# Performance work log

Measured on AMD Instinct MI355X. Metric: run time of the kernel, lower is better.

Reference implementation:

```python
import jax, jax.numpy as jnp
import numpy as np

ORIG_IN = 4096
ORIG_OUT = 4096
ACTIVE = 2048
RANK = 16
SCALING = 32.0 / 16.0  # lora_alpha / r


def setup_inputs() -> dict:
    key = jax.random.key(0)
    ks = jax.random.split(key, 7)
    x = jax.random.normal(ks[0], (2, 4096, ORIG_IN), dtype=jnp.float32)
    W_base = jax.random.normal(ks[1], (ACTIVE, ACTIVE), dtype=jnp.float32) * 0.02
    b_base = jax.random.normal(ks[2], (ACTIVE,), dtype=jnp.float32) * 0.02
    lora_A = jax.random.normal(ks[3], (RANK, ACTIVE), dtype=jnp.float32) * 0.02
    # lora_B is zero-initialized in the module, but use small random values so
    # the LoRA path contributes non-trivially to the baseline computation.
    lora_B = jax.random.normal(ks[4], (ACTIVE, RANK), dtype=jnp.float32) * 0.02
    # sorted unique index subsets (pruning masks)
    in_indices = jnp.sort(jax.random.permutation(ks[5], ORIG_IN)[:ACTIVE]).astype(jnp.int32)
    out_indices = jnp.sort(jax.random.permutation(ks[6], ORIG_OUT)[:ACTIVE]).astype(jnp.int32)
    return {
        "x": x, "W_base": W_base, "b_base": b_base,
        "lora_A": lora_A, "lora_B": lora_B,
        "in_indices": in_indices, "out_indices": out_indices,
    }


def reference(x, W_base, b_base, lora_A, lora_B, in_indices, out_indices):
    batch_dims = x.shape[:-1]
    x_flat = x.reshape(-1, ORIG_IN)            # [N, orig_in]
    x_sel = x_flat[:, in_indices]              # gather -> [N, active]
    # LoRA path: (x @ A^T) @ B^T * scaling  (dropout = identity, eval mode)
    lora_out = jnp.einsum('na,ra->nr', x_sel, lora_A)
    lora_out = jnp.einsum('nr,or->no', lora_out, lora_B) * SCALING
    # Base pruned linear
    base_out = jnp.einsum('na,oa->no', x_sel, W_base) + b_base
    combined = base_out + lora_out             # [N, active]
    # Scatter into zero-initialized full output
    out_flat = jnp.zeros((x_flat.shape[0], ORIG_OUT), dtype=combined.dtype)
    out_flat = out_flat.at[:, out_indices].set(combined)
    return out_flat.reshape(batch_dims + (ORIG_OUT,))
```

## Files before the change

### kernel.cpp

```cpp
#include <hip/hip_runtime.h>
#include <hip/hip_bf16.h>
#include <stdint.h>

#define M_DIM 8192
#define K_DIM 2048
#define N_DIM 2048
#define IN_DIM 4096
#define OUT_DIM 4096
#define SCALING 2.0f

typedef __attribute__((ext_vector_type(8))) short bf16x8_t;
typedef __attribute__((ext_vector_type(4))) float f32x4_t;

__device__ __forceinline__ void load_lds16(const void* gptr, void* lptr) {
    __builtin_amdgcn_global_load_lds(
        (const __attribute__((address_space(1))) uint32_t*)(uintptr_t)gptr,
        (__attribute__((address_space(3))) uint32_t*)(uintptr_t)lptr,
        16, 0, 0);
}

__global__ void fold_w_kernel(const float* __restrict__ Wb,
                              const float* __restrict__ lA,
                              const float* __restrict__ lB,
                              __hip_bfloat16* __restrict__ We) {
    const int k = blockIdx.x * 256 + threadIdx.x;
    const int o = blockIdx.y;
    float acc = Wb[(size_t)o * K_DIM + k];
    #pragma unroll
    for (int r = 0; r < 16; ++r)
        acc += SCALING * lB[o * 16 + r] * lA[r * K_DIM + k];
    We[(size_t)o * K_DIM + k] = __float2bfloat16(acc);
}

__global__ void gather_cast_kernel(const float* __restrict__ x,
                                   const int* __restrict__ idx,
                                   __hip_bfloat16* __restrict__ xs) {
    const int n = blockIdx.x;
    const int c0 = threadIdx.x * 8;
    const float* xrow = x + (size_t)n * IN_DIM;
    int4 i0 = *(const int4*)(idx + c0);
    int4 i1 = *(const int4*)(idx + c0 + 4);
    union { bf16x8_t v; __hip_bfloat16 h[8]; } u;
    u.h[0] = __float2bfloat16(xrow[i0.x]);
    u.h[1] = __float2bfloat16(xrow[i0.y]);
    u.h[2] = __float2bfloat16(xrow[i0.z]);
    u.h[3] = __float2bfloat16(xrow[i0.w]);
    u.h[4] = __float2bfloat16(xrow[i1.x]);
    u.h[5] = __float2bfloat16(xrow[i1.y]);
    u.h[6] = __float2bfloat16(xrow[i1.z]);
    u.h[7] = __float2bfloat16(xrow[i1.w]);
    *(bf16x8_t*)(xs + (size_t)n * K_DIM + c0) = u.v;
}

__global__ void __launch_bounds__(256, 2)
gemm_scatter_kernel(const __hip_bfloat16* __restrict__ A,
                    const __hip_bfloat16* __restrict__ B,
                    const float* __restrict__ bias,
                    const int* __restrict__ oidx,
                    float* __restrict__ out)
{
    __shared__ __hip_bfloat16 As[128 * 64];
    __shared__ __hip_bfloat16 Bs[128 * 64];

    const int tid  = threadIdx.x;
    const int wave = tid >> 6;
    const int lane = tid & 63;
    const int m0 = blockIdx.y * 128;
    const int n0 = blockIdx.x * 128;

    const int wm = (wave >> 1) * 64;
    const int wn = (wave & 1) * 64;

    const int srow  = tid >> 3;
    const int sslot = tid & 7;

    const int r15 = lane & 15;
    const int qd  = lane >> 4;

    f32x4_t acc[4][4] = {};

    for (int k0 = 0; k0 < K_DIM; k0 += 64) {
        #pragma unroll
        for (int it = 0; it < 4; ++it) {
            const int row = it * 32 + srow;
            const int q = sslot ^ (row & 7);
            const __hip_bfloat16* ga = A + (size_t)(m0 + row) * K_DIM + k0 + q * 8;
            const __hip_bfloat16* gb = B + (size_t)(n0 + row) * K_DIM + k0 + q * 8;
            load_lds16(ga, (void*)&As[(it * 32 + wave * 8) * 64]);
            load_lds16(gb, (void*)&Bs[(it * 32 + wave * 8) * 64]);
        }
        __syncthreads();

        #pragma unroll
        for (int s = 0; s < 2; ++s) {
            bf16x8_t af[4], bfr[4];
            #pragma unroll
            for (int i = 0; i < 4; ++i) {
                const int rowa = wm + i * 16 + r15;
                const int pa = (s * 4 + qd) ^ (rowa & 7);
                af[i] = *(const bf16x8_t*)&As[rowa * 64 + pa * 8];
                const int rowb = wn + i * 16 + r15;
                const int pb = (s * 4 + qd) ^ (rowb & 7);
                bfr[i] = *(const bf16x8_t*)&Bs[rowb * 64 + pb * 8];
            }
            #pragma unroll
            for (int i = 0; i < 4; ++i)
                #pragma unroll
                for (int j = 0; j < 4; ++j)
                    acc[i][j] = __builtin_amdgcn_mfma_f32_16x16x32_bf16(
                        af[i], bfr[j], acc[i][j], 0, 0, 0);
        }
        __syncthreads();
    }

    #pragma unroll
    for (int j = 0; j < 4; ++j) {
        const int gn = n0 + wn + j * 16 + r15;
        const int oc = oidx[gn];
        const float bv = bias[gn];
        #pragma unroll
        for (int i = 0; i < 4; ++i) {
            const int gm = m0 + wm + i * 16 + qd * 4;
            #pragma unroll
            for (int r = 0; r < 4; ++r)
                out[(size_t)(gm + r) * OUT_DIM + oc] = acc[i][j][r] + bv;
        }
    }
}

extern "C" void kernel_launch(void* const* d_in, const int* in_sizes, int n_in,
                              void* d_out, int out_size, void* d_ws, size_t ws_size,
                              hipStream_t stream) {
    const float* x      = (const float*)d_in[0];
    const float* W_base = (const float*)d_in[1];
    const float* b_base = (const float*)d_in[2];
    const float* lora_A = (const float*)d_in[3];
    const float* lora_B = (const float*)d_in[4];
    const int* in_idx   = (const int*)d_in[5];
    const int* out_idx  = (const int*)d_in[6];
    float* out = (float*)d_out;

    __hip_bfloat16* xs = (__hip_bfloat16*)d_ws;
    __hip_bfloat16* We = (__hip_bfloat16*)((char*)d_ws + (size_t)M_DIM * K_DIM * 2);

    hipMemsetAsync(d_out, 0, (size_t)M_DIM * OUT_DIM * sizeof(float), stream);

    fold_w_kernel<<<dim3(K_DIM / 256, N_DIM), 256, 0, stream>>>(W_base, lora_A, lora_B, We);
    gather_cast_kernel<<<M_DIM, 256, 0, stream>>>(x, in_idx, xs);
    gemm_scatter_kernel<<<dim3(N_DIM / 128, M_DIM / 128), 256, 0, stream>>>(
        xs, We, b_base, out_idx, out);
}
```

Baseline: 371.7 us.

## Write compact bf16 GEMM output then scatter via inverse index map, dropping memset

The GEMM now writes its result into a compact bf16 buffer instead of scattering fp32 values directly into the wide output. A new kernel builds an inverse column map by binary search, and a scatter kernel writes every output element exactly once with coalesced float4 stores, inserting zeros for unmapped columns. This removes the full-output memset and the strided scattered stores. The gather kernel also stages each input row into LDS with coalesced loads before indexing. The cost is an extra bf16 round-trip of the result, which also lowers output precision, and the old path remains as a fallback when workspace is too small.

```diff
diff --git a/kernel.cpp b/kernel.cpp
--- a/kernel.cpp
+++ b/kernel.cpp
@@ -32,32 +32,53 @@
     We[(size_t)o * K_DIM + k] = __float2bfloat16(acc);
 }
 
-__global__ void gather_cast_kernel(const float* __restrict__ x,
-                                   const int* __restrict__ idx,
-                                   __hip_bfloat16* __restrict__ xs) {
+__global__ void __launch_bounds__(256)
+gather_cast_kernel(const float* __restrict__ x,
+                   const int* __restrict__ idx,
+                   __hip_bfloat16* __restrict__ xs) {
+    __shared__ float row[IN_DIM];
     const int n = blockIdx.x;
+    const float* xrow = x + (size_t)n * IN_DIM;
+    #pragma unroll
+    for (int i = 0; i < 4; ++i) {
+        const int c = (i * 256 + threadIdx.x) * 4;
+        *(float4*)&row[c] = *(const float4*)&xrow[c];
+    }
+    __syncthreads();
     const int c0 = threadIdx.x * 8;
-    const float* xrow = x + (size_t)n * IN_DIM;
     int4 i0 = *(const int4*)(idx + c0);
     int4 i1 = *(const int4*)(idx + c0 + 4);
     union { bf16x8_t v; __hip_bfloat16 h[8]; } u;
-    u.h[0] = __float2bfloat16(xrow[i0.x]);
-    u.h[1] = __float2bfloat16(xrow[i0.y]);
-    u.h[2] = __float2bfloat16(xrow[i0.z]);
-    u.h[3] = __float2bfloat16(xrow[i0.w]);
-    u.h[4] = __float2bfloat16(xrow[i1.x]);
-    u.h[5] = __float2bfloat16(xrow[i1.y]);
-    u.h[6] = __float2bfloat16(xrow[i1.z]);
-    u.h[7] = __float2bfloat16(xrow[i1.w]);
+    u.h[0] = __float2bfloat16(row[i0.x]);
+    u.h[1] = __float2bfloat16(row[i0.y]);
+    u.h[2] = __float2bfloat16(row[i0.z]);
+    u.h[3] = __float2bfloat16(row[i0.w]);
+    u.h[4] = __float2bfloat16(row[i1.x]);
+    u.h[5] = __float2bfloat16(row[i1.y]);
+    u.h[6] = __float2bfloat16(row[i1.z]);
+    u.h[7] = __float2bfloat16(row[i1.w]);
     *(bf16x8_t*)(xs + (size_t)n * K_DIM + c0) = u.v;
 }
 
+__global__ void build_inv_kernel(const int* __restrict__ oidx,
+                                 int* __restrict__ inv) {
+    const int c = blockIdx.x * 256 + threadIdx.x;
+    int lo = 0, hi = N_DIM;
+    while (lo < hi) {
+        const int mid = (lo + hi) >> 1;
+        if (oidx[mid] < c) lo = mid + 1; else hi = mid;
+    }
+    inv[c] = (lo < N_DIM && oidx[lo] == c) ? lo : -1;
+}
+
+template <bool COMPACT>
 __global__ void __launch_bounds__(256, 2)
-gemm_scatter_kernel(const __hip_bfloat16* __restrict__ A,
-                    const __hip_bfloat16* __restrict__ B,
-                    const float* __restrict__ bias,
-                    const int* __restrict__ oidx,
-                    float* __restrict__ out)
+gemm_kernel(const __hip_bfloat16* __restrict__ A,
+            const __hip_bfloat16* __restrict__ B,
+            const float* __restrict__ bias,
+            const int* __restrict__ oidx,
+            float* __restrict__ out,
+            __hip_bfloat16* __restrict__ Cc)
 {
     __shared__ __hip_bfloat16 As[128 * 64];
     __shared__ __hip_bfloat16 Bs[128 * 64];
@@ -116,16 +137,43 @@
     #pragma unroll
     for (int j = 0; j < 4; ++j) {
         const int gn = n0 + wn + j * 16 + r15;
-        const int oc = oidx[gn];
         const float bv = bias[gn];
-        #pragma unroll
-        for (int i = 0; i < 4; ++i) {
-            const int gm = m0 + wm + i * 16 + qd * 4;
-            #pragma unroll
-            for (int r = 0; r < 4; ++r)
-                out[(size_t)(gm + r) * OUT_DIM + oc] = acc[i][j][r] + bv;
+        if (COMPACT) {
+            #pragma unroll
+            for (int i = 0; i < 4; ++i) {
+                const int gm = m0 + wm + i * 16 + qd * 4;
+                #pragma unroll
+                for (int r = 0; r < 4; ++r)
+                    Cc[(size_t)(gm + r) * N_DIM + gn] =
+                        __float2bfloat16(acc[i][j][r] + bv);
+            }
+        } else {
+            const int oc = oidx[gn];
+            #pragma unroll
+            for (int i = 0; i < 4; ++i) {
+                const int gm = m0 + wm + i * 16 + qd * 4;
+                #pragma unroll
+                for (int r = 0; r < 4; ++r)
+                    out[(size_t)(gm + r) * OUT_DIM + oc] = acc[i][j][r] + bv;
+            }
         }
     }
+}
+
+__global__ void __launch_bounds__(256)
+scatter_out_kernel(const __hip_bfloat16* __restrict__ C,
+                   const int* __restrict__ inv,
+                   float* __restrict__ out) {
+    const int row = blockIdx.y;
+    const int c0 = (blockIdx.x * 256 + threadIdx.x) * 4;
+    const __hip_bfloat16* crow = C + (size_t)row * N_DIM;
+    const int4 iv = *(const int4*)(inv + c0);
+    float4 v;
+    v.x = (iv.x >= 0) ? __bfloat162float(crow[iv.x]) : 0.0f;
+    v.y = (iv.y >= 0) ? __bfloat162float(crow[iv.y]) : 0.0f;
+    v.z = (iv.z >= 0) ? __bfloat162float(crow[iv.z]) : 0.0f;
+    v.w = (iv.w >= 0) ? __bfloat162float(crow[iv.w]) : 0.0f;
+    *(float4*)(out + (size_t)row * OUT_DIM + c0) = v;
 }
 
 extern "C" void kernel_launch(void* const* d_in, const int* in_sizes, int n_in,
@@ -140,13 +188,28 @@
     const int* out_idx  = (const int*)d_in[6];
     float* out = (float*)d_out;
 
+    const size_t sz_xs = (size_t)M_DIM * K_DIM * 2;
+    const size_t sz_We = (size_t)N_DIM * K_DIM * 2;
+    const size_t sz_C  = (size_t)M_DIM * N_DIM * 2;
+    const size_t sz_inv = (size_t)OUT_DIM * 4;
+
     __hip_bfloat16* xs = (__hip_bfloat16*)d_ws;
-    __hip_bfloat16* We = (__hip_bfloat16*)((char*)d_ws + (size_t)M_DIM * K_DIM * 2);
-
-    hipMemsetAsync(d_out, 0, (size_t)M_DIM * OUT_DIM * sizeof(float), stream);
+    __hip_bfloat16* We = (__hip_bfloat16*)((char*)d_ws + sz_xs);
+    __hip_bfloat16* Cc = (__hip_bfloat16*)((char*)d_ws + sz_xs + sz_We);
+    int* inv           = (int*)((char*)d_ws + sz_xs + sz_We + sz_C);
 
     fold_w_kernel<<<dim3(K_DIM / 256, N_DIM), 256, 0, stream>>>(W_base, lora_A, lora_B, We);
     gather_cast_kernel<<<M_DIM, 256, 0, stream>>>(x, in_idx, xs);
-    gemm_scatter_kernel<<<dim3(N_DIM / 128, M_DIM / 128), 256, 0, stream>>>(
-        xs, We, b_base, out_idx, out);
-}
+
+    if (ws_size >= sz_xs + sz_We + sz_C + sz_inv) {
+        build_inv_kernel<<<OUT_DIM / 256, 256, 0, stream>>>(out_idx, inv);
+        gemm_kernel<true><<<dim3(N_DIM / 128, M_DIM / 128), 256, 0, stream>>>(
+            xs, We, b_base, out_idx, out, Cc);
+        scatter_out_kernel<<<dim3(OUT_DIM / (256 * 4), M_DIM), 256, 0, stream>>>(
+            Cc, inv, out);
+    } else {
+        hipMemsetAsync(d_out, 0, (size_t)M_DIM * OUT_DIM * sizeof(float), stream);
+        gemm_kernel<false><<<dim3(N_DIM / 128, M_DIM / 128), 256, 0, stream>>>(
+            xs, We, b_base, out_idx, out, Cc);
+    }
+}
```

New measurement: 345.2 us. -7.1%, faster.
